# Performance work log

Measured on AMD Instinct MI355X. Metric: run time of the kernel, lower is better.

## Reference

```python
import jax, jax.numpy as jnp
import numpy as np

OUT = 7          # output_size
SR = 2           # sampling_ratio
SCALES = (0.25, 0.125, 0.0625, 0.03125)
K_MIN, K_MAX = 2, 5   # -log2(scales[0]), -log2(scales[-1])
CANON_SCALE, CANON_LVL, EPS = 224.0, 4.0, 1e-6


def _roi_align_level(feat, b_idx, boxes, scale):
    """ROIAlign (maskrcnn-benchmark, non-aligned) of all boxes on one level.
    feat: [B,C,H,W], b_idx: [N] int, boxes: [N,4] xyxy in image coords.
    Returns [N,C,OUT,OUT]."""
    N = boxes.shape[0]
    H, W = feat.shape[2], feat.shape[3]
    x1 = boxes[:, 0] * scale
    y1 = boxes[:, 1] * scale
    x2 = boxes[:, 2] * scale
    y2 = boxes[:, 3] * scale
    roi_w = jnp.maximum(x2 - x1, 1.0)
    roi_h = jnp.maximum(y2 - y1, 1.0)
    bin_w = roi_w / OUT
    bin_h = roi_h / OUT
    # sample positions inside each bin, in bin units: [OUT*SR]
    sub = (jnp.arange(SR, dtype=feat.dtype) + 0.5) / SR
    grid1d = (jnp.arange(OUT, dtype=feat.dtype)[:, None] + sub[None, :]).reshape(-1)
    ys = y1[:, None] + bin_h[:, None] * grid1d[None, :]   # [N, OUT*SR]
    xs = x1[:, None] + bin_w[:, None] * grid1d[None, :]   # [N, OUT*SR]
    K = OUT * SR
    Yf = jnp.broadcast_to(ys[:, :, None], (N, K, K)).reshape(N, K * K)
    Xf = jnp.broadcast_to(xs[:, None, :], (N, K, K)).reshape(N, K * K)
    valid = (Yf >= -1.0) & (Yf <= H) & (Xf >= -1.0) & (Xf <= W)
    y = jnp.clip(Yf, 0.0, H - 1)
    x = jnp.clip(Xf, 0.0, W - 1)
    y0 = jnp.floor(y).astype(jnp.int32)
    x0 = jnp.floor(x).astype(jnp.int32)
    y1i = jnp.minimum(y0 + 1, H - 1)
    x1i = jnp.minimum(x0 + 1, W - 1)
    ly = y - y0
    lx = x - x0
    hy = 1.0 - ly
    hx = 1.0 - lx
    b = b_idx[:, None]  # [N,1] broadcasts with [N,K*K]
    def g(yi, xi):
        return feat[b, :, yi, xi]  # [N, K*K, C]
    val = (g(y0, x0) * (hy * hx)[..., None]
           + g(y0, x1i) * (hy * lx)[..., None]
           + g(y1i, x0) * (ly * hx)[..., None]
           + g(y1i, x1i) * (ly * lx)[..., None])
    val = jnp.where(valid[..., None], val, 0.0)
    # [N, OUT, SR, OUT, SR, C] -> average sampling points -> [N, OUT, OUT, C]
    val = val.reshape(N, OUT, SR, OUT, SR, -1).mean(axis=(2, 4))
    return jnp.transpose(val, (0, 3, 1, 2))  # [N, C, OUT, OUT]


def _map_levels(boxes):
    # BoxList.area with TO_REMOVE = 1 (xyxy mode)
    area = (boxes[:, 2] - boxes[:, 0] + 1.0) * (boxes[:, 3] - boxes[:, 1] + 1.0)
    s = jnp.sqrt(area)
    lvl = jnp.floor(CANON_LVL + jnp.log2(s / CANON_SCALE + EPS))
    lvl = jnp.clip(lvl, K_MIN, K_MAX)
    return lvl.astype(jnp.int32) - K_MIN  # 0..3


def setup_inputs() -> dict:
    key = jax.random.key(0)
    ks = jax.random.split(key, 10)
    N = 1024
    H_img, W_img = 800.0, 1216.0
    x1 = jax.random.uniform(ks[0], (N,), minval=0.0, maxval=W_img - 64.0)
    y1 = jax.random.uniform(ks[1], (N,), minval=0.0, maxval=H_img - 64.0)
    w = jax.random.uniform(ks[2], (N,), minval=8.0, maxval=500.0)
    h = jax.random.uniform(ks[3], (N,), minval=8.0, maxval=500.0)
    x2 = jnp.minimum(x1 + w, W_img - 1.0)
    y2 = jnp.minimum(y1 + h, H_img - 1.0)
    boxes = jnp.stack([x1, y1, x2, y2], axis=1).astype(jnp.float32)
    box_batch_idx = jnp.sort(jax.random.randint(ks[4], (N,), 0, 2)).astype(jnp.int32)
    f0 = jax.random.normal(ks[5], (2, 256, 200, 304), dtype=jnp.float32)
    f1 = jax.random.normal(ks[6], (2, 256, 100, 152), dtype=jnp.float32)
    f2 = jax.random.normal(ks[7], (2, 256, 50, 76), dtype=jnp.float32)
    f3 = jax.random.normal(ks[8], (2, 256, 25, 38), dtype=jnp.float32)
    return {"f0": f0, "f1": f1, "f2": f2, "f3": f3,
            "boxes": boxes, "box_batch_idx": box_batch_idx}


def reference(f0, f1, f2, f3, boxes, box_batch_idx):
    feats = (f0, f1, f2, f3)
    levels = _map_levels(boxes)  # [N] in 0..3
    out = None
    for lvl, (feat, scale) in enumerate(zip(feats, SCALES)):
        pooled = _roi_align_level(feat, box_batch_idx, boxes, scale)
        mask = (levels == lvl)[:, None, None, None]
        part = jnp.where(mask, pooled, 0.0)
        out = part if out is None else out + part
    return out  # [N, C, OUT, OUT]
```

## Files before the change

kernel.cpp:

```cpp
#include <hip/hip_runtime.h>
#include <math.h>

#define TILE_F 1792
#define HALF_F 896
#define MAXI  7
#define MAXIP 4
#define MAXK3 6

typedef __attribute__((address_space(3))) void lds_void;
typedef const __attribute__((address_space(1))) void g_void;

__device__ __forceinline__ void dma16(const float* g, float* l) {
  __builtin_amdgcn_global_load_lds((g_void*)g, (lds_void*)l, 16, 0, 0);
}
__device__ __forceinline__ void dma4(const float* g, float* l) {
  __builtin_amdgcn_global_load_lds((g_void*)g, (lds_void*)l, 4, 0, 0);
}
__device__ __forceinline__ void wait_vmcnt(int k) {
  switch (k) {
    case 0: asm volatile("s_waitcnt vmcnt(0)" ::: "memory"); break;
    case 1: asm volatile("s_waitcnt vmcnt(1)" ::: "memory"); break;
    case 2: asm volatile("s_waitcnt vmcnt(2)" ::: "memory"); break;
    case 3: asm volatile("s_waitcnt vmcnt(3)" ::: "memory"); break;
    case 4: asm volatile("s_waitcnt vmcnt(4)" ::: "memory"); break;
    case 5: asm volatile("s_waitcnt vmcnt(5)" ::: "memory"); break;
    default: asm volatile("s_waitcnt vmcnt(6)" ::: "memory"); break;
  }
}

#define COMPUTE_STORE(TP, CC)                                                  \
  if (lane < 49) {                                                             \
    float acc = 0.0f;                                                          \
    _Pragma("unroll")                                                          \
    for (int sy = 0; sy < 2; ++sy) {                                           \
      _Pragma("unroll")                                                        \
      for (int sx = 0; sx < 2; ++sx) {                                         \
        const float w00 = (TP)[rT[sy] + Cc0[sx]];                              \
        const float w01 = (TP)[rT[sy] + Cc1[sx]];                              \
        const float w10 = (TP)[rB[sy] + Cc0[sx]];                              \
        const float w11 = (TP)[rB[sy] + Cc1[sx]];                              \
        const float bil = HY[sy] * (HX[sx] * w00 + LX[sx] * w01)               \
                        + LY[sy] * (HX[sx] * w10 + LX[sx] * w11);              \
        acc += (VY[sy] * VX[sx]) * bil;                                        \
      }                                                                        \
    }                                                                          \
    outp[(CC) * 49] = acc * 0.25f;                                             \
  }

__global__ __launch_bounds__(128) void pooler_kernel(
    const float* __restrict__ f0, const float* __restrict__ f1,
    const float* __restrict__ f2, const float* __restrict__ f3,
    const float* __restrict__ boxes, const int* __restrict__ bidx,
    float* __restrict__ out, int N)
{
  __shared__ __align__(16) float tile[2][TILE_F];
  const int tid  = threadIdx.x;
  const int wave = tid >> 6, lane = tid & 63;
  const int n    = blockIdx.y;
  if (n >= N) return;

  const float bx1 = boxes[4*n+0], by1 = boxes[4*n+1];
  const float bx2 = boxes[4*n+2], by2 = boxes[4*n+3];
  const float area = (bx2 - bx1 + 1.0f) * (by2 - by1 + 1.0f);
  const float s    = sqrtf(area);
  int lvl = (int)floorf(4.0f + log2f(s / 224.0f + 1e-6f));
  lvl = lvl < 2 ? 2 : (lvl > 5 ? 5 : lvl);
  const int li = lvl - 2;

  int H, W; const float* feat; float scale;
  switch (li) {
    case 0:  feat = f0; H = 200; W = 304; scale = 0.25f;    break;
    case 1:  feat = f1; H = 100; W = 152; scale = 0.125f;   break;
    case 2:  feat = f2; H = 50;  W = 76;  scale = 0.0625f;  break;
    default: feat = f3; H = 25;  W = 38;  scale = 0.03125f; break;
  }
  const int b = bidx[n];
  const float x1s = bx1 * scale, y1s = by1 * scale;
  const float roiw = fmaxf(bx2 * scale - x1s, 1.0f);
  const float roih = fmaxf(by2 * scale - y1s, 1.0f);
  const float binw = roiw / 7.0f, binh = roih / 7.0f;
  const float Hm1f = (float)(H - 1), Wm1f = (float)(W - 1);
  const int   Hm1  = H - 1,          Wm1  = W - 1;

  const float yA = fminf(fmaxf(y1s + binh * 0.25f, 0.0f), Hm1f);
  const float yB = fminf(fmaxf(y1s + binh * 6.75f, 0.0f), Hm1f);
  const float xA = fminf(fmaxf(x1s + binw * 0.25f, 0.0f), Wm1f);
  const float xB = fminf(fmaxf(x1s + binw * 6.75f, 0.0f), Wm1f);
  const int y_lo  = (int)yA;
  const int y_hi  = min((int)yB + 1, Hm1);
  const int regH  = y_hi - y_lo + 1;
  const int x_lo4 = ((int)xA) & ~3;
  const int x_hi  = min((int)xB + 1, Wm1);
  const int row4  = ((x_hi - x_lo4 + 4) >> 2);
  const int regW4 = row4 << 2;

  const int bin = (lane < 49) ? lane : 0;
  const int ph = bin / 7, pw = bin - (bin / 7) * 7;
  int   rT[2], rB[2], Cc0[2], Cc1[2];
  float HY[2], LY[2], VY[2], HX[2], LX[2], VX[2];
#pragma unroll
  for (int t = 0; t < 2; ++t) {
    {
      const float g  = (float)ph + 0.25f + 0.5f * (float)t;
      const float Yf = y1s + binh * g;
      VY[t] = (Yf >= -1.0f && Yf <= (float)H) ? 1.0f : 0.0f;
      const float y = fminf(fmaxf(Yf, 0.0f), Hm1f);
      const int  y0 = (int)y;
      LY[t] = y - (float)y0;  HY[t] = 1.0f - LY[t];
      rT[t] = (y0 - y_lo) * regW4;
      rB[t] = (min(y0 + 1, Hm1) - y_lo) * regW4;
    }
    {
      const float g  = (float)pw + 0.25f + 0.5f * (float)t;
      const float Xf = x1s + binw * g;
      VX[t] = (Xf >= -1.0f && Xf <= (float)W) ? 1.0f : 0.0f;
      const float x = fminf(fmaxf(Xf, 0.0f), Wm1f);
      const int  x0 = (int)x;
      LX[t] = x - (float)x0;  HX[t] = 1.0f - LX[t];
      Cc0[t] = x0 - x_lo4;
      Cc1[t] = min(x0 + 1, Wm1) - x_lo4;
    }
  }

  const size_t planeHW = (size_t)H * W;
  const int    cbase   = (blockIdx.x << 5) + (wave << 4);
  const float* plane0  = feat + ((size_t)(b * 256 + cbase)) * planeHW
                              + (size_t)y_lo * W;
  float*       outp    = out + ((size_t)n * 256 + cbase) * 49 + lane;
  float*       myt     = tile[wave];

  if (li != 3) {
    int cnt4 = regH * row4;
    if (cnt4 > TILE_F / 4) cnt4 = TILE_F / 4;

    if (cnt4 <= HALF_F / 4) {
      int soff[MAXIP];
#pragma unroll
      for (int i = 0; i < MAXIP; ++i) {
        const int u = lane + (i << 6);
        if (u < cnt4) {
          const int r = u / row4;
          const int c = u - r * row4;
          soff[i] = r * W + x_lo4 + (c << 2);
        } else soff[i] = -1;
      }
      const int K = (cnt4 + 63) >> 6;

#pragma unroll
      for (int i = 0; i < MAXIP; ++i)
        if (soff[i] >= 0) dma16(plane0 + soff[i], myt + (i << 8));

      for (int cc = 0; cc < 16; ++cc) {
        asm volatile("s_waitcnt lgkmcnt(0)" ::: "memory");
        if (cc < 15) {
          const float* planeN = plane0 + (size_t)(cc + 1) * planeHW;
          float* bufN = myt + ((cc & 1) ? 0 : HALF_F);
#pragma unroll
          for (int i = 0; i < MAXIP; ++i)
            if (soff[i] >= 0) dma16(planeN + soff[i], bufN + (i << 8));
          wait_vmcnt(K);
        } else {
          asm volatile("s_waitcnt vmcnt(0)" ::: "memory");
        }
        const float* bufC = myt + ((cc & 1) ? HALF_F : 0);
        COMPUTE_STORE(bufC, cc)
      }
    } else {
      int soff[MAXI];
#pragma unroll
      for (int i = 0; i < MAXI; ++i) {
        const int u = lane + (i << 6);
        if (u < cnt4) {
          const int r = u / row4;
          const int c = u - r * row4;
          soff[i] = r * W + x_lo4 + (c << 2);
        } else soff[i] = -1;
      }
      for (int cc = 0; cc < 16; ++cc) {
        const float* plane = plane0 + (size_t)cc * planeHW;
        asm volatile("s_waitcnt lgkmcnt(0)" ::: "memory");
#pragma unroll
        for (int i = 0; i < MAXI; ++i)
          if (soff[i] >= 0) dma16(plane + soff[i], myt + (i << 8));
        asm volatile("s_waitcnt vmcnt(0)" ::: "memory");
        COMPUTE_STORE(myt, cc)
      }
    }
  } else {
    int cntS = regH * regW4;
    if (cntS > (MAXK3 << 6)) cntS = MAXK3 << 6;
    int soff3[MAXK3];
#pragma unroll
    for (int k = 0; k < MAXK3; ++k) {
      const int u = (k << 6) + lane;
      if (u < cntS) {
        const int r   = u / regW4;
        const int c   = u - r * regW4;
        const int col = x_lo4 + c;
        soff3[k] = (col <= Wm1) ? (r * W + col) : -1;
      } else soff3[k] = -1;
    }
    const int K3 = (cntS + 63) >> 6;

#pragma unroll
    for (int k = 0; k < MAXK3; ++k)
      if (soff3[k] >= 0) dma4(plane0 + soff3[k], myt + (k << 6));

    for (int cc = 0; cc < 16; ++cc) {
      asm volatile("s_waitcnt lgkmcnt(0)" ::: "memory");
      if (cc < 15) {
        const float* planeN = plane0 + (size_t)(cc + 1) * planeHW;
        float* bufN = myt + ((cc & 1) ? 0 : HALF_F);
#pragma unroll
        for (int k = 0; k < MAXK3; ++k)
          if (soff3[k] >= 0) dma4(planeN + soff3[k], bufN + (k << 6));
        wait_vmcnt(K3);
      } else {
        asm volatile("s_waitcnt vmcnt(0)" ::: "memory");
      }
      const float* bufC = myt + ((cc & 1) ? HALF_F : 0);
      COMPUTE_STORE(bufC, cc)
    }
  }
}

extern "C" void kernel_launch(void* const* d_in, const int* in_sizes, int n_in,
                              void* d_out, int out_size, void* d_ws, size_t ws_size,
                              hipStream_t stream) {
  const float* f0    = (const float*)d_in[0];
  const float* f1    = (const float*)d_in[1];
  const float* f2    = (const float*)d_in[2];
  const float* f3    = (const float*)d_in[3];
  const float* boxes = (const float*)d_in[4];
  const int*   bidx  = (const int*)d_in[5];
  const int N = in_sizes[5];
  dim3 grid(8, N);
  pooler_kernel<<<grid, 128, 0, stream>>>(f0, f1, f2, f3, boxes, bidx,
                                          (float*)d_out, N);
}
```

Baseline: 285.0 us.

## Halve channels per block and add 4-stage LDS prefetch for small regions

Doubles the grid to 16 blocks per ROI so each wave handles 8 channels instead of 16, raising parallelism. Small-footprint regions (level 3 and small tiles) now use a 4-buffer ring with three planes in flight instead of double buffering, so more memory latency is hidden. The cost is more blocks with repeated per-ROI setup and a shorter loop over which the prefetch ramp is amortized.

```diff
diff --git a/kernel.cpp b/kernel.cpp
--- a/kernel.cpp
+++ b/kernel.cpp
@@ -2,10 +2,13 @@
 #include <math.h>
 
 #define TILE_F 1792
-#define HALF_F 896
-#define MAXI  7
-#define MAXIP 4
-#define MAXK3 6
+#define B448   448
+#define B896   896
+#define NCH    8
+#define MAXI   7
+#define MAXIP  4
+#define MAXI4  2
+#define MAXK3  6
 
 typedef __attribute__((address_space(3))) void lds_void;
 typedef const __attribute__((address_space(1))) void g_void;
@@ -18,13 +21,25 @@
 }
 __device__ __forceinline__ void wait_vmcnt(int k) {
   switch (k) {
-    case 0: asm volatile("s_waitcnt vmcnt(0)" ::: "memory"); break;
-    case 1: asm volatile("s_waitcnt vmcnt(1)" ::: "memory"); break;
-    case 2: asm volatile("s_waitcnt vmcnt(2)" ::: "memory"); break;
-    case 3: asm volatile("s_waitcnt vmcnt(3)" ::: "memory"); break;
-    case 4: asm volatile("s_waitcnt vmcnt(4)" ::: "memory"); break;
-    case 5: asm volatile("s_waitcnt vmcnt(5)" ::: "memory"); break;
-    default: asm volatile("s_waitcnt vmcnt(6)" ::: "memory"); break;
+    case 0:  asm volatile("s_waitcnt vmcnt(0)"  ::: "memory"); break;
+    case 1:  asm volatile("s_waitcnt vmcnt(1)"  ::: "memory"); break;
+    case 2:  asm volatile("s_waitcnt vmcnt(2)"  ::: "memory"); break;
+    case 3:  asm volatile("s_waitcnt vmcnt(3)"  ::: "memory"); break;
+    case 4:  asm volatile("s_waitcnt vmcnt(4)"  ::: "memory"); break;
+    case 5:  asm volatile("s_waitcnt vmcnt(5)"  ::: "memory"); break;
+    case 6:  asm volatile("s_waitcnt vmcnt(6)"  ::: "memory"); break;
+    case 7:  asm volatile("s_waitcnt vmcnt(7)"  ::: "memory"); break;
+    case 8:  asm volatile("s_waitcnt vmcnt(8)"  ::: "memory"); break;
+    case 9:  asm volatile("s_waitcnt vmcnt(9)"  ::: "memory"); break;
+    case 10: asm volatile("s_waitcnt vmcnt(10)" ::: "memory"); break;
+    case 11: asm volatile("s_waitcnt vmcnt(11)" ::: "memory"); break;
+    case 12: asm volatile("s_waitcnt vmcnt(12)" ::: "memory"); break;
+    case 13: asm volatile("s_waitcnt vmcnt(13)" ::: "memory"); break;
+    case 14: asm volatile("s_waitcnt vmcnt(14)" ::: "memory"); break;
+    case 15: asm volatile("s_waitcnt vmcnt(15)" ::: "memory"); break;
+    case 16: asm volatile("s_waitcnt vmcnt(16)" ::: "memory"); break;
+    case 17: asm volatile("s_waitcnt vmcnt(17)" ::: "memory"); break;
+    default: asm volatile("s_waitcnt vmcnt(18)" ::: "memory"); break;
   }
 }
 
@@ -123,7 +138,7 @@
   }
 
   const size_t planeHW = (size_t)H * W;
-  const int    cbase   = (blockIdx.x << 5) + (wave << 4);
+  const int    cbase   = (blockIdx.x << 4) + (wave << 3);
   const float* plane0  = feat + ((size_t)(b * 256 + cbase)) * planeHW
                               + (size_t)y_lo * W;
   float*       outp    = out + ((size_t)n * 256 + cbase) * 49 + lane;
@@ -133,7 +148,43 @@
     int cnt4 = regH * row4;
     if (cnt4 > TILE_F / 4) cnt4 = TILE_F / 4;
 
-    if (cnt4 <= HALF_F / 4) {
+    if (cnt4 <= B448 / 4) {
+      int soff[MAXI4];
+#pragma unroll
+      for (int i = 0; i < MAXI4; ++i) {
+        const int u = lane + (i << 6);
+        if (u < cnt4) {
+          const int r = u / row4;
+          const int c = u - r * row4;
+          soff[i] = r * W + x_lo4 + (c << 2);
+        } else soff[i] = -1;
+      }
+      const int K = (cnt4 + 63) >> 6;
+
+#pragma unroll
+      for (int p = 0; p < 3; ++p) {
+        const float* pl = plane0 + (size_t)p * planeHW;
+        float* bf = myt + p * B448;
+#pragma unroll
+        for (int i = 0; i < MAXI4; ++i)
+          if (soff[i] >= 0) dma16(pl + soff[i], bf + (i << 8));
+      }
+
+      for (int cc = 0; cc < NCH; ++cc) {
+        asm volatile("s_waitcnt lgkmcnt(0)" ::: "memory");
+        if (cc + 3 < NCH) {
+          const float* pl = plane0 + (size_t)(cc + 3) * planeHW;
+          float* bf = myt + ((cc + 3) & 3) * B448;
+#pragma unroll
+          for (int i = 0; i < MAXI4; ++i)
+            if (soff[i] >= 0) dma16(pl + soff[i], bf + (i << 8));
+        }
+        const int rem = NCH - 1 - cc;
+        wait_vmcnt(K * (rem > 3 ? 3 : rem));
+        const float* bufC = myt + (cc & 3) * B448;
+        COMPUTE_STORE(bufC, cc)
+      }
+    } else if (cnt4 <= B896 / 4) {
       int soff[MAXIP];
 #pragma unroll
       for (int i = 0; i < MAXIP; ++i) {
@@ -150,19 +201,19 @@
       for (int i = 0; i < MAXIP; ++i)
         if (soff[i] >= 0) dma16(plane0 + soff[i], myt + (i << 8));
 
-      for (int cc = 0; cc < 16; ++cc) {
+      for (int cc = 0; cc < NCH; ++cc) {
         asm volatile("s_waitcnt lgkmcnt(0)" ::: "memory");
-        if (cc < 15) {
-          const float* planeN = plane0 + (size_t)(cc + 1) * planeHW;
-          float* bufN = myt + ((cc & 1) ? 0 : HALF_F);
+        if (cc + 1 < NCH) {
+          const float* pl = plane0 + (size_t)(cc + 1) * planeHW;
+          float* bf = myt + ((cc + 1) & 1) * B896;
 #pragma unroll
           for (int i = 0; i < MAXIP; ++i)
-            if (soff[i] >= 0) dma16(planeN + soff[i], bufN + (i << 8));
+            if (soff[i] >= 0) dma16(pl + soff[i], bf + (i << 8));
           wait_vmcnt(K);
         } else {
           asm volatile("s_waitcnt vmcnt(0)" ::: "memory");
         }
-        const float* bufC = myt + ((cc & 1) ? HALF_F : 0);
+        const float* bufC = myt + (cc & 1) * B896;
         COMPUTE_STORE(bufC, cc)
       }
     } else {
@@ -176,7 +227,7 @@
           soff[i] = r * W + x_lo4 + (c << 2);
         } else soff[i] = -1;
       }
-      for (int cc = 0; cc < 16; ++cc) {
+      for (int cc = 0; cc < NCH; ++cc) {
         const float* plane = plane0 + (size_t)cc * planeHW;
         asm volatile("s_waitcnt lgkmcnt(0)" ::: "memory");
 #pragma unroll
@@ -203,22 +254,26 @@
     const int K3 = (cntS + 63) >> 6;
 
 #pragma unroll
-    for (int k = 0; k < MAXK3; ++k)
-      if (soff3[k] >= 0) dma4(plane0 + soff3[k], myt + (k << 6));
-
-    for (int cc = 0; cc < 16; ++cc) {
+    for (int p = 0; p < 3; ++p) {
+      const float* pl = plane0 + (size_t)p * planeHW;
+      float* bf = myt + p * B448;
+#pragma unroll
+      for (int k = 0; k < MAXK3; ++k)
+        if (soff3[k] >= 0) dma4(pl + soff3[k], bf + (k << 6));
+    }
+
+    for (int cc = 0; cc < NCH; ++cc) {
       asm volatile("s_waitcnt lgkmcnt(0)" ::: "memory");
-      if (cc < 15) {
-        const float* planeN = plane0 + (size_t)(cc + 1) * planeHW;
-        float* bufN = myt + ((cc & 1) ? 0 : HALF_F);
+      if (cc + 3 < NCH) {
+        const float* pl = plane0 + (size_t)(cc + 3) * planeHW;
+        float* bf = myt + ((cc + 3) & 3) * B448;
 #pragma unroll
         for (int k = 0; k < MAXK3; ++k)
-          if (soff3[k] >= 0) dma4(planeN + soff3[k], bufN + (k << 6));
-        wait_vmcnt(K3);
-      } else {
-        asm volatile("s_waitcnt vmcnt(0)" ::: "memory");
-      }
-      const float* bufC = myt + ((cc & 1) ? HALF_F : 0);
+          if (soff3[k] >= 0) dma4(pl + soff3[k], bf + (k << 6));
+      }
+      const int rem = NCH - 1 - cc;
+      wait_vmcnt(K3 * (rem > 3 ? 3 : rem));
+      const float* bufC = myt + (cc & 3) * B448;
       COMPUTE_STORE(bufC, cc)
     }
   }
@@ -234,7 +289,7 @@
   const float* boxes = (const float*)d_in[4];
   const int*   bidx  = (const int*)d_in[5];
   const int N = in_sizes[5];
-  dim3 grid(8, N);
+  dim3 grid(16, N);
   pooler_kernel<<<grid, 128, 0, stream>>>(f0, f1, f2, f3, boxes, bidx,
                                           (float*)d_out, N);
 }
```

Result: faster. 279.0 us (-2.1%).
